# Performance work log

Measured on AMD Instinct MI355X. Metric: run time of the kernel, lower is better.

The kernel has to match this reference:

```python
import jax, jax.numpy as jnp
import numpy as np

BS, H = 2048, 1024
XDIM = 2048 + 4 * 64  # x + R*W = 2304
IN = XDIM + 2 * H     # 4352


def setup_inputs() -> dict:
    key = jax.random.key(0)
    ks = jax.random.split(key, 11)
    s = 1.0 / np.sqrt(IN)  # torch Linear default init scale
    return {
        "input_x": jax.random.normal(ks[0], (BS, XDIM), jnp.float32),
        "previous_time": jax.random.normal(ks[1], (BS, H), jnp.float32),
        "previous_layer": jax.random.normal(ks[2], (BS, H), jnp.float32),
        "old_state": jnp.zeros((BS, H), jnp.float32),
        "Wi": jax.random.normal(ks[3], (H, IN), jnp.float32) * s,
        "bi": jax.random.normal(ks[4], (H,), jnp.float32) * s,
        "Wf": jax.random.normal(ks[5], (H, IN), jnp.float32) * s,
        "bf": jax.random.normal(ks[6], (H,), jnp.float32) * s,
        "Wo": jax.random.normal(ks[7], (H, IN), jnp.float32) * s,
        "bo": jax.random.normal(ks[8], (H,), jnp.float32) * s,
        "Ws": jax.random.normal(ks[9], (H, IN), jnp.float32) * s,
        "bs_state": jax.random.normal(ks[10], (H,), jnp.float32) * s,
    }


def reference(input_x, previous_time, previous_layer, old_state,
              Wi, bi, Wf, bf, Wo, bo, Ws, bs_state):
    # semicolon_input: [bs, x + R*W + 2h]
    z = jnp.concatenate([input_x, previous_time, previous_layer], axis=1)
    # Fuse the four projections into one GEMM: [bs, 4h]
    W_all = jnp.concatenate([Wi, Wf, Wo, Ws], axis=0)          # [4h, IN]
    b_all = jnp.concatenate([bi, bf, bo, bs_state], axis=0)    # [4h]
    proj = z @ W_all.T + b_all
    gi, gf, go, gs = jnp.split(proj, 4, axis=1)
    input_gate = jax.nn.sigmoid(gi)
    forget_gate = jax.nn.sigmoid(gf)
    output_gate = jax.nn.sigmoid(go)
    new_state = forget_gate * old_state + input_gate * jnp.tanh(gs)
    new_hidden = output_gate * jnp.tanh(new_state)
    return new_hidden
```

## Files before the change

### kernel.cpp

```cpp
#include <hip/hip_runtime.h>
#include <stdint.h>
#include <stddef.h>

#define M_DIM 2048
#define N_DIM 4096
#define K_DIM 4352
#define H_DIM 1024
#define X_DIM 2304

#define A_OFF 0u
#define B_OFF 17825792u
#define P_OFF 53477376u

typedef __bf16 bf16x8 __attribute__((ext_vector_type(8)));
typedef float f32x4 __attribute__((ext_vector_type(4)));

__device__ __forceinline__ unsigned short f32_to_bf16(float f) {
    unsigned u = __float_as_uint(f);
    u += 0x7FFFu + ((u >> 16) & 1u);
    return (unsigned short)(u >> 16);
}

__global__ __launch_bounds__(256) void convert_kernel(
    const float* __restrict__ x, const float* __restrict__ pt,
    const float* __restrict__ pl,
    const float* __restrict__ Wi, const float* __restrict__ Wf,
    const float* __restrict__ Wo, const float* __restrict__ Ws,
    unsigned short* __restrict__ Abf, unsigned short* __restrict__ Bbf)
{
    int col4 = blockIdx.x * 256 + threadIdx.x;
    if (col4 >= K_DIM / 4) return;
    int col = col4 * 4;
    int row = blockIdx.y;

    const float* src;
    unsigned short* dst;
    if (row < M_DIM) {
        if (col < X_DIM)             src = x  + (size_t)row * X_DIM + col;
        else if (col < X_DIM + H_DIM) src = pt + (size_t)row * H_DIM + (col - X_DIM);
        else                          src = pl + (size_t)row * H_DIM + (col - X_DIM - H_DIM);
        dst = Abf + (size_t)row * K_DIM + col;
    } else {
        int n = row - M_DIM;
        const float* W = (n < 1024) ? Wi : (n < 2048) ? Wf : (n < 3072) ? Wo : Ws;
        src = W + (size_t)(n & 1023) * K_DIM + col;
        dst = Bbf + (size_t)n * K_DIM + col;
    }
    float4 v = *(const float4*)src;
    union { unsigned short h[4]; uint64_t u; } r;
    r.h[0] = f32_to_bf16(v.x);
    r.h[1] = f32_to_bf16(v.y);
    r.h[2] = f32_to_bf16(v.z);
    r.h[3] = f32_to_bf16(v.w);
    *(uint64_t*)dst = r.u;
}

__global__ __launch_bounds__(256) void gemm_bt(
    const unsigned short* __restrict__ A,
    const unsigned short* __restrict__ B,
    float* __restrict__ C)
{
    __shared__ unsigned short sA[128 * 64];
    __shared__ unsigned short sB[128 * 64];

    const int tid  = threadIdx.x;
    const int lane = tid & 63;
    const int wave = tid >> 6;
    const int wm = (wave >> 1) * 64;
    const int wn = (wave & 1) * 64;
    const int m0 = blockIdx.y * 128;
    const int n0 = blockIdx.x * 128;

    const int srow = tid >> 3;
    const int scol = (tid & 7) * 8;

    const int fr = lane & 15;
    const int fk = (lane >> 4) * 8;

    f32x4 acc[4][4];
#pragma unroll
    for (int i = 0; i < 4; ++i)
#pragma unroll
        for (int j = 0; j < 4; ++j) acc[i][j] = (f32x4){0.f, 0.f, 0.f, 0.f};

    const unsigned short* Ab = A + (size_t)(m0 + srow) * K_DIM + scol;
    const unsigned short* Bb = B + (size_t)(n0 + srow) * K_DIM + scol;

    for (int kt = 0; kt < K_DIM; kt += 64) {
        __syncthreads();
#pragma unroll
        for (int i = 0; i < 4; ++i) {
            __builtin_amdgcn_global_load_lds(
                (const __attribute__((address_space(1))) unsigned*)(Ab + (size_t)i * 32 * K_DIM + kt),
                (__attribute__((address_space(3))) unsigned*)((char*)sA + i * 4096 + wave * 1024),
                16, 0, 0);
            __builtin_amdgcn_global_load_lds(
                (const __attribute__((address_space(1))) unsigned*)(Bb + (size_t)i * 32 * K_DIM + kt),
                (__attribute__((address_space(3))) unsigned*)((char*)sB + i * 4096 + wave * 1024),
                16, 0, 0);
        }
        __syncthreads();

#pragma unroll
        for (int kk = 0; kk < 64; kk += 32) {
            bf16x8 af[4], bfr[4];
#pragma unroll
            for (int i = 0; i < 4; ++i) {
                af[i]  = *(const bf16x8*)(sA + (wm + i * 16 + fr) * 64 + kk + fk);
                bfr[i] = *(const bf16x8*)(sB + (wn + i * 16 + fr) * 64 + kk + fk);
            }
#pragma unroll
            for (int i = 0; i < 4; ++i)
#pragma unroll
                for (int j = 0; j < 4; ++j)
                    acc[i][j] = __builtin_amdgcn_mfma_f32_16x16x32_bf16(
                        af[i], bfr[j], acc[i][j], 0, 0, 0);
        }
    }

    const int crow = m0 + wm + (lane >> 4) * 4;
    const int ccol = n0 + wn + (lane & 15);
#pragma unroll
    for (int i = 0; i < 4; ++i)
#pragma unroll
        for (int j = 0; j < 4; ++j) {
            float* cp = C + (size_t)(crow + i * 16) * N_DIM + (ccol + j * 16);
#pragma unroll
            for (int r = 0; r < 4; ++r) cp[(size_t)r * N_DIM] = acc[i][j][r];
        }
}

__device__ __forceinline__ float sigm_(float x) { return 1.f / (1.f + __expf(-x)); }
__device__ __forceinline__ float tanh_(float x) {
    x = fminf(15.f, fmaxf(-15.f, x));
    float e = __expf(2.f * x);
    return (e - 1.f) / (e + 1.f);
}

__global__ __launch_bounds__(256) void epilogue_kernel(
    const float* __restrict__ proj,
    const float* __restrict__ old_state,
    const float* __restrict__ bi, const float* __restrict__ bfv,
    const float* __restrict__ bo, const float* __restrict__ bs,
    float* __restrict__ out)
{
    int idx = blockIdx.x * 256 + threadIdx.x;
    int m  = idx >> 8;
    int h4 = idx & 255;

    const float4* prow = (const float4*)(proj + (size_t)m * N_DIM);
    float4 gi = prow[h4];
    float4 gf = prow[256 + h4];
    float4 go = prow[512 + h4];
    float4 gs = prow[768 + h4];
    float4 vbi = ((const float4*)bi)[h4];
    float4 vbf = ((const float4*)bfv)[h4];
    float4 vbo = ((const float4*)bo)[h4];
    float4 vbs = ((const float4*)bs)[h4];
    float4 old = ((const float4*)old_state)[(size_t)m * 256 + h4];

    float4 o;
    {
        float ig = sigm_(gi.x + vbi.x), fg = sigm_(gf.x + vbf.x);
        float og = sigm_(go.x + vbo.x), ts = tanh_(gs.x + vbs.x);
        o.x = og * tanh_(fg * old.x + ig * ts);
    }
    {
        float ig = sigm_(gi.y + vbi.y), fg = sigm_(gf.y + vbf.y);
        float og = sigm_(go.y + vbo.y), ts = tanh_(gs.y + vbs.y);
        o.y = og * tanh_(fg * old.y + ig * ts);
    }
    {
        float ig = sigm_(gi.z + vbi.z), fg = sigm_(gf.z + vbf.z);
        float og = sigm_(go.z + vbo.z), ts = tanh_(gs.z + vbs.z);
        o.z = og * tanh_(fg * old.z + ig * ts);
    }
    {
        float ig = sigm_(gi.w + vbi.w), fg = sigm_(gf.w + vbf.w);
        float og = sigm_(go.w + vbo.w), ts = tanh_(gs.w + vbs.w);
        o.w = og * tanh_(fg * old.w + ig * ts);
    }
    ((float4*)out)[(size_t)m * 256 + h4] = o;
}

extern "C" void kernel_launch(void* const* d_in, const int* in_sizes, int n_in,
                              void* d_out, int out_size, void* d_ws, size_t ws_size,
                              hipStream_t stream) {
    const float* x   = (const float*)d_in[0];
    const float* pt  = (const float*)d_in[1];
    const float* pl  = (const float*)d_in[2];
    const float* old = (const float*)d_in[3];
    const float* Wi  = (const float*)d_in[4];
    const float* bi  = (const float*)d_in[5];
    const float* Wf  = (const float*)d_in[6];
    const float* bf  = (const float*)d_in[7];
    const float* Wo  = (const float*)d_in[8];
    const float* bo  = (const float*)d_in[9];
    const float* Ws  = (const float*)d_in[10];
    const float* bs  = (const float*)d_in[11];
    float* out = (float*)d_out;

    char* ws = (char*)d_ws;
    unsigned short* Abf = (unsigned short*)(ws + A_OFF);
    unsigned short* Bbf = (unsigned short*)(ws + B_OFF);
    float*          prj = (float*)(ws + P_OFF);

    dim3 cgrid((K_DIM / 4 + 255) / 256, M_DIM + N_DIM);
    convert_kernel<<<cgrid, 256, 0, stream>>>(x, pt, pl, Wi, Wf, Wo, Ws, Abf, Bbf);

    dim3 ggrid(N_DIM / 128, M_DIM / 128);
    gemm_bt<<<ggrid, 256, 0, stream>>>(Abf, Bbf, prj);

    epilogue_kernel<<<(M_DIM * H_DIM / 4) / 256, 256, 0, stream>>>(
        prj, old, bi, bf, bo, bs, out);
}
```

Baseline: 266.6 us.

## Fuse LSTM gate epilogue into GEMM via interleaved weight rows

Weight rows are reordered during conversion so the four gates for each hidden unit sit in adjacent columns (h*4+g). This lets each GEMM tile compute all gates for 32 hidden units and apply the sigmoid/tanh cell update directly from shared memory, which removes the 32 MB fp32 projection round-trip and the separate epilogue launch. The GEMM also moves to 512 threads with 2x4 MFMA tiles per wave, and the convert kernel now handles one row per block with 8-wide stores. The costs are more shared memory for the staging buffer, extra barriers in the epilogue, and scalar (non-vector) output stores.

```diff
diff --git a/kernel.cpp b/kernel.cpp
--- a/kernel.cpp
+++ b/kernel.cpp
@@ -10,7 +10,6 @@
 
 #define A_OFF 0u
 #define B_OFF 17825792u
-#define P_OFF 53477376u
 
 typedef __bf16 bf16x8 __attribute__((ext_vector_type(8)));
 typedef float f32x4 __attribute__((ext_vector_type(4)));
@@ -19,6 +18,13 @@
     unsigned u = __float_as_uint(f);
     u += 0x7FFFu + ((u >> 16) & 1u);
     return (unsigned short)(u >> 16);
+}
+
+__device__ __forceinline__ float sigm_(float x) { return 1.f / (1.f + __expf(-x)); }
+__device__ __forceinline__ float tanh_(float x) {
+    x = fminf(15.f, fmaxf(-15.f, x));
+    float e = __expf(2.f * x);
+    return (e - 1.f) / (e + 1.f);
 }
 
 __global__ __launch_bounds__(256) void convert_kernel(
@@ -28,159 +34,144 @@
     const float* __restrict__ Wo, const float* __restrict__ Ws,
     unsigned short* __restrict__ Abf, unsigned short* __restrict__ Bbf)
 {
-    int col4 = blockIdx.x * 256 + threadIdx.x;
-    if (col4 >= K_DIM / 4) return;
-    int col = col4 * 4;
-    int row = blockIdx.y;
-
-    const float* src;
-    unsigned short* dst;
+    const int row = blockIdx.x;
+    const float* srow;
+    unsigned short* drow;
+    int src_extent;
     if (row < M_DIM) {
-        if (col < X_DIM)             src = x  + (size_t)row * X_DIM + col;
-        else if (col < X_DIM + H_DIM) src = pt + (size_t)row * H_DIM + (col - X_DIM);
-        else                          src = pl + (size_t)row * H_DIM + (col - X_DIM - H_DIM);
-        dst = Abf + (size_t)row * K_DIM + col;
+        drow = Abf + (size_t)row * K_DIM;
+        srow = nullptr; src_extent = 0;
     } else {
         int n = row - M_DIM;
-        const float* W = (n < 1024) ? Wi : (n < 2048) ? Wf : (n < 3072) ? Wo : Ws;
-        src = W + (size_t)(n & 1023) * K_DIM + col;
-        dst = Bbf + (size_t)n * K_DIM + col;
-    }
-    float4 v = *(const float4*)src;
-    union { unsigned short h[4]; uint64_t u; } r;
-    r.h[0] = f32_to_bf16(v.x);
-    r.h[1] = f32_to_bf16(v.y);
-    r.h[2] = f32_to_bf16(v.z);
-    r.h[3] = f32_to_bf16(v.w);
-    *(uint64_t*)dst = r.u;
-}
-
-__global__ __launch_bounds__(256) void gemm_bt(
+        int g = n >> 10, h = n & 1023;
+        const float* W = (g == 0) ? Wi : (g == 1) ? Wf : (g == 2) ? Wo : Ws;
+        srow = W + (size_t)h * K_DIM;
+        drow = Bbf + (size_t)(h * 4 + g) * K_DIM;
+        src_extent = K_DIM;
+    }
+
+    for (int c8 = threadIdx.x; c8 < K_DIM / 8; c8 += 256) {
+        int col = c8 * 8;
+        const float* s;
+        if (row < M_DIM) {
+            if (col < X_DIM)              s = x  + (size_t)row * X_DIM + col;
+            else if (col < X_DIM + H_DIM) s = pt + (size_t)row * H_DIM + (col - X_DIM);
+            else                          s = pl + (size_t)row * H_DIM + (col - X_DIM - H_DIM);
+        } else {
+            s = srow + col;
+        }
+        float4 v0 = ((const float4*)s)[0];
+        float4 v1 = ((const float4*)s)[1];
+        union { unsigned short h[8]; uint4 u; } r;
+        r.h[0] = f32_to_bf16(v0.x); r.h[1] = f32_to_bf16(v0.y);
+        r.h[2] = f32_to_bf16(v0.z); r.h[3] = f32_to_bf16(v0.w);
+        r.h[4] = f32_to_bf16(v1.x); r.h[5] = f32_to_bf16(v1.y);
+        r.h[6] = f32_to_bf16(v1.z); r.h[7] = f32_to_bf16(v1.w);
+        *(uint4*)(drow + col) = r.u;
+    }
+}
+
+__global__ __launch_bounds__(512, 4) void gemm_fused(
     const unsigned short* __restrict__ A,
     const unsigned short* __restrict__ B,
-    float* __restrict__ C)
-{
-    __shared__ unsigned short sA[128 * 64];
-    __shared__ unsigned short sB[128 * 64];
-
-    const int tid  = threadIdx.x;
-    const int lane = tid & 63;
-    const int wave = tid >> 6;
-    const int wm = (wave >> 1) * 64;
-    const int wn = (wave & 1) * 64;
-    const int m0 = blockIdx.y * 128;
-    const int n0 = blockIdx.x * 128;
-
-    const int srow = tid >> 3;
-    const int scol = (tid & 7) * 8;
-
-    const int fr = lane & 15;
-    const int fk = (lane >> 4) * 8;
-
-    f32x4 acc[4][4];
-#pragma unroll
-    for (int i = 0; i < 4; ++i)
-#pragma unroll
-        for (int j = 0; j < 4; ++j) acc[i][j] = (f32x4){0.f, 0.f, 0.f, 0.f};
-
-    const unsigned short* Ab = A + (size_t)(m0 + srow) * K_DIM + scol;
-    const unsigned short* Bb = B + (size_t)(n0 + srow) * K_DIM + scol;
-
-    for (int kt = 0; kt < K_DIM; kt += 64) {
-        __syncthreads();
-#pragma unroll
-        for (int i = 0; i < 4; ++i) {
-            __builtin_amdgcn_global_load_lds(
-                (const __attribute__((address_space(1))) unsigned*)(Ab + (size_t)i * 32 * K_DIM + kt),
-                (__attribute__((address_space(3))) unsigned*)((char*)sA + i * 4096 + wave * 1024),
-                16, 0, 0);
-            __builtin_amdgcn_global_load_lds(
-                (const __attribute__((address_space(1))) unsigned*)(Bb + (size_t)i * 32 * K_DIM + kt),
-                (__attribute__((address_space(3))) unsigned*)((char*)sB + i * 4096 + wave * 1024),
-                16, 0, 0);
-        }
-        __syncthreads();
-
-#pragma unroll
-        for (int kk = 0; kk < 64; kk += 32) {
-            bf16x8 af[4], bfr[4];
-#pragma unroll
-            for (int i = 0; i < 4; ++i) {
-                af[i]  = *(const bf16x8*)(sA + (wm + i * 16 + fr) * 64 + kk + fk);
-                bfr[i] = *(const bf16x8*)(sB + (wn + i * 16 + fr) * 64 + kk + fk);
-            }
-#pragma unroll
-            for (int i = 0; i < 4; ++i)
-#pragma unroll
-                for (int j = 0; j < 4; ++j)
-                    acc[i][j] = __builtin_amdgcn_mfma_f32_16x16x32_bf16(
-                        af[i], bfr[j], acc[i][j], 0, 0, 0);
-        }
-    }
-
-    const int crow = m0 + wm + (lane >> 4) * 4;
-    const int ccol = n0 + wn + (lane & 15);
-#pragma unroll
-    for (int i = 0; i < 4; ++i)
-#pragma unroll
-        for (int j = 0; j < 4; ++j) {
-            float* cp = C + (size_t)(crow + i * 16) * N_DIM + (ccol + j * 16);
-#pragma unroll
-            for (int r = 0; r < 4; ++r) cp[(size_t)r * N_DIM] = acc[i][j][r];
-        }
-}
-
-__device__ __forceinline__ float sigm_(float x) { return 1.f / (1.f + __expf(-x)); }
-__device__ __forceinline__ float tanh_(float x) {
-    x = fminf(15.f, fmaxf(-15.f, x));
-    float e = __expf(2.f * x);
-    return (e - 1.f) / (e + 1.f);
-}
-
-__global__ __launch_bounds__(256) void epilogue_kernel(
-    const float* __restrict__ proj,
     const float* __restrict__ old_state,
     const float* __restrict__ bi, const float* __restrict__ bfv,
     const float* __restrict__ bo, const float* __restrict__ bs,
     float* __restrict__ out)
 {
-    int idx = blockIdx.x * 256 + threadIdx.x;
-    int m  = idx >> 8;
-    int h4 = idx & 255;
-
-    const float4* prow = (const float4*)(proj + (size_t)m * N_DIM);
-    float4 gi = prow[h4];
-    float4 gf = prow[256 + h4];
-    float4 go = prow[512 + h4];
-    float4 gs = prow[768 + h4];
-    float4 vbi = ((const float4*)bi)[h4];
-    float4 vbf = ((const float4*)bfv)[h4];
-    float4 vbo = ((const float4*)bo)[h4];
-    float4 vbs = ((const float4*)bs)[h4];
-    float4 old = ((const float4*)old_state)[(size_t)m * 256 + h4];
-
-    float4 o;
-    {
-        float ig = sigm_(gi.x + vbi.x), fg = sigm_(gf.x + vbf.x);
-        float og = sigm_(go.x + vbo.x), ts = tanh_(gs.x + vbs.x);
-        o.x = og * tanh_(fg * old.x + ig * ts);
-    }
-    {
-        float ig = sigm_(gi.y + vbi.y), fg = sigm_(gf.y + vbf.y);
-        float og = sigm_(go.y + vbo.y), ts = tanh_(gs.y + vbs.y);
-        o.y = og * tanh_(fg * old.y + ig * ts);
-    }
-    {
-        float ig = sigm_(gi.z + vbi.z), fg = sigm_(gf.z + vbf.z);
-        float og = sigm_(go.z + vbo.z), ts = tanh_(gs.z + vbs.z);
-        o.z = og * tanh_(fg * old.z + ig * ts);
-    }
-    {
-        float ig = sigm_(gi.w + vbi.w), fg = sigm_(gf.w + vbf.w);
-        float og = sigm_(go.w + vbo.w), ts = tanh_(gs.w + vbs.w);
-        o.w = og * tanh_(fg * old.w + ig * ts);
-    }
-    ((float4*)out)[(size_t)m * 256 + h4] = o;
+    __shared__ unsigned short sA[128 * 64];
+    __shared__ unsigned short sB[128 * 64];
+    __shared__ float sP[128 * 76];
+
+    const int tid  = threadIdx.x;
+    const int lane = tid & 63;
+    const int wave = tid >> 6;
+    const int wm = (wave >> 1) * 32;
+    const int wn = (wave & 1) * 64;
+    const int m0 = blockIdx.y * 128;
+    const int n0 = blockIdx.x * 128;
+
+    const int r8 = lane >> 3;
+    const int c8 = (lane & 7) * 8;
+
+    const int fr = lane & 15;
+    const int fk = (lane >> 4) * 8;
+
+    f32x4 acc[2][4];
+#pragma unroll
+    for (int i = 0; i < 2; ++i)
+#pragma unroll
+        for (int j = 0; j < 4; ++j) acc[i][j] = (f32x4){0.f, 0.f, 0.f, 0.f};
+
+    const unsigned short* Aw = A + (size_t)(m0 + wave * 8 + r8) * K_DIM + c8;
+    const unsigned short* Bw = B + (size_t)(n0 + wave * 8 + r8) * K_DIM + c8;
+
+    for (int kt = 0; kt < K_DIM; kt += 64) {
+        __syncthreads();
+#pragma unroll
+        for (int i = 0; i < 2; ++i) {
+            __builtin_amdgcn_global_load_lds(
+                (const __attribute__((address_space(1))) unsigned*)(Aw + (size_t)i * 64 * K_DIM + kt),
+                (__attribute__((address_space(3))) unsigned*)((char*)sA + (i * 8 + wave) * 1024),
+                16, 0, 0);
+            __builtin_amdgcn_global_load_lds(
+                (const __attribute__((address_space(1))) unsigned*)(Bw + (size_t)i * 64 * K_DIM + kt),
+                (__attribute__((address_space(3))) unsigned*)((char*)sB + (i * 8 + wave) * 1024),
+                16, 0, 0);
+        }
+        __syncthreads();
+
+#pragma unroll
+        for (int kk = 0; kk < 64; kk += 32) {
+            bf16x8 af[2], bfr[4];
+#pragma unroll
+            for (int i = 0; i < 2; ++i)
+                af[i] = *(const bf16x8*)(sA + (wm + i * 16 + fr) * 64 + kk + fk);
+#pragma unroll
+            for (int j = 0; j < 4; ++j)
+                bfr[j] = *(const bf16x8*)(sB + (wn + j * 16 + fr) * 64 + kk + fk);
+#pragma unroll
+            for (int i = 0; i < 2; ++i)
+#pragma unroll
+                for (int j = 0; j < 4; ++j)
+                    acc[i][j] = __builtin_amdgcn_mfma_f32_16x16x32_bf16(
+                        af[i], bfr[j], acc[i][j], 0, 0, 0);
+        }
+    }
+
+    const int cw = lane & 15;
+    const int rw = (lane >> 4) * 4;
+    const int hl = tid & 15;
+    const int rb = tid >> 4;
+
+    for (int p = 0; p < 2; ++p) {
+        __syncthreads();
+        if ((wave & 1) == p) {
+#pragma unroll
+            for (int i = 0; i < 2; ++i)
+#pragma unroll
+                for (int j = 0; j < 4; ++j)
+#pragma unroll
+                    for (int r = 0; r < 4; ++r)
+                        sP[(wm + i * 16 + rw + r) * 76 + j * 16 + cw] = acc[i][j][r];
+        }
+        __syncthreads();
+
+        const int hg = (n0 >> 2) + p * 16 + hl;
+        const float b_i = bi[hg], b_f = bfv[hg], b_o = bo[hg], b_s = bs[hg];
+#pragma unroll
+        for (int k = 0; k < 4; ++k) {
+            const int row = rb + 32 * k;
+            float4 g = *(const float4*)(sP + row * 76 + hl * 4);
+            const size_t oidx = (size_t)(m0 + row) * H_DIM + hg;
+            float old = old_state[oidx];
+            float ig = sigm_(g.x + b_i);
+            float fg = sigm_(g.y + b_f);
+            float og = sigm_(g.z + b_o);
+            float ts = tanh_(g.w + b_s);
+            out[oidx] = og * tanh_(fg * old + ig * ts);
+        }
+    }
 }
 
 extern "C" void kernel_launch(void* const* d_in, const int* in_sizes, int n_in,
@@ -203,14 +194,9 @@
     char* ws = (char*)d_ws;
     unsigned short* Abf = (unsigned short*)(ws + A_OFF);
     unsigned short* Bbf = (unsigned short*)(ws + B_OFF);
-    float*          prj = (float*)(ws + P_OFF);
-
-    dim3 cgrid((K_DIM / 4 + 255) / 256, M_DIM + N_DIM);
-    convert_kernel<<<cgrid, 256, 0, stream>>>(x, pt, pl, Wi, Wf, Wo, Ws, Abf, Bbf);
+
+    convert_kernel<<<M_DIM + N_DIM, 256, 0, stream>>>(x, pt, pl, Wi, Wf, Wo, Ws, Abf, Bbf);
 
     dim3 ggrid(N_DIM / 128, M_DIM / 128);
-    gemm_bt<<<ggrid, 256, 0, stream>>>(Abf, Bbf, prj);
-
-    epilogue_kernel<<<(M_DIM * H_DIM / 4) / 256, 256, 0, stream>>>(
-        prj, old, bi, bf, bo, bs, out);
-}
+    gemm_fused<<<ggrid, 512, 0, stream>>>(Abf, Bbf, old, bi, bf, bo, bs, out);
+}
```

Result: no change. 268.6 us (+0.8%).
